# Kernel optimization log

Measured on AMD Instinct MI355X. Metric: run time of the kernel, lower is better.

Reference implementation:

```python
import jax, jax.numpy as jnp
import numpy as np
import math

B, S, E, HEAD = 4, 2048, 1024, 64  # num_heads=16 -> head_size = 1024//16


def setup_inputs() -> dict:
    key = jax.random.key(0)
    kx, kp, kq, kk, kv = jax.random.split(key, 5)
    std = math.sqrt(2.0 / (E + HEAD))
    return {
        "x": jax.random.normal(kx, (B, S, E), dtype=jnp.float32),
        "padding_mask": jax.random.randint(kp, (B, S), 0, 2, dtype=jnp.int32),
        "Wq": jax.random.normal(kq, (HEAD, E), dtype=jnp.float32) * std,
        "Wk": jax.random.normal(kk, (HEAD, E), dtype=jnp.float32) * std,
        "Wv": jax.random.normal(kv, (HEAD, E), dtype=jnp.float32) * std,
    }


def reference(x, padding_mask, Wq, Wk, Wv):
    # q,k,v: [B,S,head] via Linear (x @ W.T, no bias)
    q = jnp.einsum("bse,he->bsh", x, Wq)
    k = jnp.einsum("bse,he->bsh", x, Wk)
    v = jnp.einsum("bse,he->bsh", x, Wv)
    scores = jnp.einsum("bqh,bkh->bqk", q, k)  # [B,S,S]
    seq = x.shape[1]
    causal = jnp.tril(jnp.ones((seq, seq), dtype=jnp.float32))  # [S,S]
    mask = causal[None, :, :] * padding_mask.astype(jnp.float32)[:, None, :]  # [B,S,S]
    scores = jnp.where(mask == 0, jnp.float32(-1e9), scores)
    head_size = k.shape[-1]
    attn = jax.nn.softmax(scores / jnp.sqrt(jnp.float32(head_size)), axis=-1)
    return jnp.einsum("bqk,bkh->bqh", attn, v)
```

## Files before the change

### kernel.cpp

```cpp
#include <hip/hip_runtime.h>
#include <hip/hip_bf16.h>
#include <math.h>

#define B_ 4
#define S_ 2048
#define E_ 1024
#define H_ 64
#define NQT 32
#define SPLITS 8
#define TPS 4

typedef short bf16x8 __attribute__((ext_vector_type(8)));
typedef float f32x4 __attribute__((ext_vector_type(4)));
typedef unsigned short u16x8 __attribute__((ext_vector_type(8)));
typedef unsigned short u16x4 __attribute__((ext_vector_type(4)));

__device__ __forceinline__ unsigned short f2bf(float f){
    unsigned u = __builtin_bit_cast(unsigned, f);
    u += 0x7fffu + ((u >> 16) & 1u);
    return (unsigned short)(u >> 16);
}
__device__ __forceinline__ float bf2f(unsigned short h){
    return __builtin_bit_cast(float, ((unsigned)h) << 16);
}
#define MFMA16(a,b,c) __builtin_amdgcn_mfma_f32_16x16x32_bf16((a),(b),(c),0,0,0)

__global__ __launch_bounds__(256) void qkv_kernel(
    const float* __restrict__ x, const float* __restrict__ Wq,
    const float* __restrict__ Wk, const float* __restrict__ Wv,
    unsigned short* __restrict__ Qhi, unsigned short* __restrict__ Qlo,
    unsigned short* __restrict__ Khi, unsigned short* __restrict__ Klo,
    unsigned short* __restrict__ Vt)
{
    __shared__ unsigned short Ah[64*64], Al[64*64], Bh[64*64], Bl[64*64];
    const int m0 = blockIdx.x * 64;
    const int comp = blockIdx.y;
    const float* W = (comp==0) ? Wq : (comp==1) ? Wk : Wv;
    const int tid = threadIdx.x;
    const int lane = tid & 63, wv = tid >> 6, l15 = lane & 15, quad = lane >> 4;

    f32x4 acc[4];
    #pragma unroll
    for (int i=0;i<4;i++) acc[i] = f32x4{0.f,0.f,0.f,0.f};

    const int arow = tid >> 2;
    const int ag0  = (tid & 3) * 2;

    for (int k0 = 0; k0 < E_; k0 += 64) {
        const float* xs = x + (size_t)(m0 + arow)*E_ + k0 + ag0*8;
        float4 xa = ((const float4*)xs)[0];
        float4 xb = ((const float4*)xs)[1];
        float4 xc = ((const float4*)xs)[2];
        float4 xd = ((const float4*)xs)[3];
        const float* wsrc = W + (size_t)arow*E_ + k0 + ag0*8;
        float4 wa = ((const float4*)wsrc)[0];
        float4 wb = ((const float4*)wsrc)[1];
        float4 wc = ((const float4*)wsrc)[2];
        float4 wd = ((const float4*)wsrc)[3];
        __syncthreads();
        auto put = [&](unsigned short* hi_t, unsigned short* lo_t, int g, float4 p, float4 q2){
            u16x8 hv, lv;
            float vv[8] = {p.x,p.y,p.z,p.w,q2.x,q2.y,q2.z,q2.w};
            #pragma unroll
            for (int j=0;j<8;j++){ unsigned short h = f2bf(vv[j]); hv[j]=h; lv[j]=f2bf(vv[j]-bf2f(h)); }
            int idx = arow*8 + (g ^ (arow & 7));
            ((u16x8*)hi_t)[idx] = hv; ((u16x8*)lo_t)[idx] = lv;
        };
        put(Ah, Al, ag0,   xa, xb);
        put(Ah, Al, ag0+1, xc, xd);
        put(Bh, Bl, ag0,   wa, wb);
        put(Bh, Bl, ag0+1, wc, wd);
        __syncthreads();
        #pragma unroll
        for (int kk=0; kk<2; kk++){
            const int arw = wv*16 + l15;
            bf16x8 ah = ((const bf16x8*)Ah)[arw*8 + ((kk*4+quad) ^ (l15 & 7))];
            bf16x8 al = ((const bf16x8*)Al)[arw*8 + ((kk*4+quad) ^ (l15 & 7))];
            #pragma unroll
            for (int nt=0; nt<4; nt++){
                const int brw = nt*16 + l15;
                bf16x8 bh = ((const bf16x8*)Bh)[brw*8 + ((kk*4+quad) ^ (l15 & 7))];
                bf16x8 bl = ((const bf16x8*)Bl)[brw*8 + ((kk*4+quad) ^ (l15 & 7))];
                acc[nt] = MFMA16(ah, bh, acc[nt]);
                acc[nt] = MFMA16(ah, bl, acc[nt]);
                acc[nt] = MFMA16(al, bh, acc[nt]);
            }
        }
    }
    if (comp < 2) {
        unsigned short* dh = (comp==0) ? Qhi : Khi;
        unsigned short* dl = (comp==0) ? Qlo : Klo;
        #pragma unroll
        for (int nt=0; nt<4; nt++)
        #pragma unroll
        for (int r=0; r<4; r++){
            int row = m0 + wv*16 + quad*4 + r;
            float v = acc[nt][r];
            unsigned short h = f2bf(v);
            dh[(size_t)row*H_ + nt*16 + l15] = h;
            dl[(size_t)row*H_ + nt*16 + l15] = f2bf(v - bf2f(h));
        }
    } else {
        int b = m0 >> 11;
        int s0 = (m0 & (S_-1)) + wv*16 + quad*4;
        #pragma unroll
        for (int nt=0; nt<4; nt++){
            u16x4 pk;
            #pragma unroll
            for (int r=0;r<4;r++) pk[r] = f2bf(acc[nt][r]);
            *(u16x4*)(Vt + (size_t)b*H_*S_ + (size_t)(nt*16+l15)*S_ + s0) = pk;
        }
    }
}

__global__ __launch_bounds__(256) void meanv_kernel(const unsigned short* __restrict__ Vt,
                                                    float* __restrict__ meanV)
{
    int b = blockIdx.x >> 6, h = blockIdx.x & 63;
    const unsigned short* src = Vt + (size_t)b*H_*S_ + (size_t)h*S_;
    float sum = 0.f;
    for (int j = threadIdx.x; j < S_; j += 256) sum += bf2f(src[j]);
    #pragma unroll
    for (int m=32; m>=1; m>>=1) sum += __shfl_xor(sum, m);
    __shared__ float red[4];
    if ((threadIdx.x & 63) == 0) red[threadIdx.x >> 6] = sum;
    __syncthreads();
    if (threadIdx.x == 0) meanV[b*H_ + h] = (red[0]+red[1]+red[2]+red[3]) * (1.f/S_);
}

__global__ __launch_bounds__(256) void attn_kernel(
    const unsigned short* __restrict__ Qhi, const unsigned short* __restrict__ Qlo,
    const unsigned short* __restrict__ Khi, const unsigned short* __restrict__ Klo,
    const unsigned short* __restrict__ Vt, const int* __restrict__ pad,
    float* __restrict__ Opart, float* __restrict__ mpart, float* __restrict__ lpart)
{
    const int qt = blockIdx.x, b = blockIdx.y, sp = blockIdx.z;
    const int t0 = sp * TPS;
    if (t0 > qt) return;
    const int t1 = min(t0 + TPS, qt + 1);

    __shared__ unsigned short KtH[64*64], KtL[64*64], Vts[64*64];
    __shared__ unsigned short Ps[4][64*20];
    __shared__ int pad_s[64];

    const int tid = threadIdx.x, lane = tid & 63, wv = tid >> 6, l15 = lane & 15, quad = lane >> 4;
    const int role = tid >> 6, srow = tid & 63;

    const size_t qrow = (size_t)(b*S_ + qt*64 + wv*16 + l15);
    bf16x8 aqh0 = *(const bf16x8*)(Qhi + qrow*H_ + quad*8);
    bf16x8 aqh1 = *(const bf16x8*)(Qhi + qrow*H_ + 32 + quad*8);
    bf16x8 aql0 = *(const bf16x8*)(Qlo + qrow*H_ + quad*8);
    bf16x8 aql1 = *(const bf16x8*)(Qlo + qrow*H_ + 32 + quad*8);

    float m_i[4], l_i[4];
    f32x4 o[4];
    #pragma unroll
    for (int r=0;r<4;r++){ m_i[r] = -INFINITY; l_i[r] = 0.f; }
    #pragma unroll
    for (int i=0;i<4;i++) o[i] = f32x4{0.f,0.f,0.f,0.f};

    const int qg = qt*64 + wv*16 + quad*4;
    unsigned short* Pw = &Ps[wv][0];

    for (int t = t0; t < t1; ++t) {
        const int kb = t * 64;
        __syncthreads();
        if (role < 3) {
            const unsigned short* gs =
                (role==0) ? (Khi + ((size_t)(b*S_ + kb + srow))*H_) :
                (role==1) ? (Klo + ((size_t)(b*S_ + kb + srow))*H_) :
                            (Vt + (size_t)b*H_*S_ + (size_t)srow*S_ + kb);
            unsigned short* ld = (role==0) ? KtH : (role==1) ? KtL : Vts;
            #pragma unroll
            for (int i=0;i<8;i++){
                u16x8 d = ((const u16x8*)gs)[i];
                ((u16x8*)ld)[srow*8 + (i ^ (srow & 7))] = d;
            }
        } else {
            pad_s[srow] = pad[b*S_ + kb + srow];
        }
        __syncthreads();

        f32x4 s[4];
        #pragma unroll
        for (int nt=0; nt<4; nt++){
            const int krw = nt*16 + l15;
            bf16x8 bh0 = ((const bf16x8*)KtH)[krw*8 + ((quad)   ^ (l15 & 7))];
            bf16x8 bh1 = ((const bf16x8*)KtH)[krw*8 + ((4+quad) ^ (l15 & 7))];
            bf16x8 bl0 = ((const bf16x8*)KtL)[krw*8 + ((quad)   ^ (l15 & 7))];
            bf16x8 bl1 = ((const bf16x8*)KtL)[krw*8 + ((4+quad) ^ (l15 & 7))];
            f32x4 z = f32x4{0.f,0.f,0.f,0.f};
            z = MFMA16(aqh0, bh0, z);
            z = MFMA16(aqh1, bh1, z);
            z = MFMA16(aqh0, bl0, z);
            z = MFMA16(aqh1, bl1, z);
            z = MFMA16(aql0, bh0, z);
            z = MFMA16(aql1, bh1, z);
            s[nt] = z;
        }
        float rmax[4] = {-INFINITY,-INFINITY,-INFINITY,-INFINITY};
        #pragma unroll
        for (int nt=0; nt<4; nt++){
            const int kcol = nt*16 + l15;
            const int kg = kb + kcol;
            const int pv = pad_s[kcol];
            #pragma unroll
            for (int r=0;r<4;r++){
                bool ok = (kg <= qg + r) && (pv != 0);
                float v = ok ? s[nt][r]*0.125f : -1.25e8f;
                s[nt][r] = v;
                rmax[r] = fmaxf(rmax[r], v);
            }
        }
        #pragma unroll
        for (int msk=1; msk<=8; msk<<=1){
            #pragma unroll
            for (int r=0;r<4;r++) rmax[r] = fmaxf(rmax[r], __shfl_xor(rmax[r], msk));
        }
        float alpha[4];
        #pragma unroll
        for (int r=0;r<4;r++){
            float mn = fmaxf(m_i[r], rmax[r]);
            alpha[r] = __expf(m_i[r] - mn);
            m_i[r] = mn;
        }
        float rsum[4] = {0.f,0.f,0.f,0.f};
        #pragma unroll
        for (int nt=0; nt<4; nt++)
        #pragma unroll
        for (int r=0;r<4;r++){
            float p = __expf(s[nt][r] - m_i[r]);
            s[nt][r] = p;
            rsum[r] += p;
        }
        #pragma unroll
        for (int msk=1; msk<=8; msk<<=1){
            #pragma unroll
            for (int r=0;r<4;r++) rsum[r] += __shfl_xor(rsum[r], msk);
        }
        #pragma unroll
        for (int r=0;r<4;r++) l_i[r] = l_i[r]*alpha[r] + rsum[r];
        #pragma unroll
        for (int hnt=0; hnt<4; hnt++)
        #pragma unroll
        for (int r=0;r<4;r++) o[hnt][r] *= alpha[r];

        #pragma unroll
        for (int nt=0; nt<4; nt++){
            const int key = nt*16 + l15;
            u16x4 pk;
            #pragma unroll
            for (int r=0;r<4;r++) pk[r] = f2bf(s[nt][r]);
            *(u16x4*)(Pw + key*20 + quad*4) = pk;
        }
        #pragma unroll
        for (int ks=0; ks<2; ks++){
            bf16x8 ap;
            #pragma unroll
            for (int j=0;j<8;j++) ap[j] = (short)Pw[(ks*32 + quad*8 + j)*20 + l15];
            #pragma unroll
            for (int hnt=0; hnt<4; hnt++){
                bf16x8 bv = ((const bf16x8*)Vts)[(hnt*16+l15)*8 + ((ks*4+quad) ^ (l15 & 7))];
                o[hnt] = MFMA16(ap, bv, o[hnt]);
            }
        }
    }
    const size_t rbase = ((size_t)((b*NQT + qt)*SPLITS + sp))*64 + wv*16 + quad*4;
    if (l15 == 0) {
        #pragma unroll
        for (int r=0;r<4;r++){ mpart[rbase + r] = m_i[r]; lpart[rbase + r] = l_i[r]; }
    }
    #pragma unroll
    for (int hnt=0; hnt<4; hnt++)
    #pragma unroll
    for (int r=0;r<4;r++)
        Opart[(rbase + r)*H_ + hnt*16 + l15] = o[hnt][r];
}

__global__ __launch_bounds__(256) void combine_kernel(
    const float* __restrict__ Opart, const float* __restrict__ mpart,
    const float* __restrict__ lpart, const float* __restrict__ meanV,
    float* __restrict__ out)
{
    const int idx = blockIdx.x*256 + threadIdx.x;
    const int h = idx & 63;
    const int q = (idx >> 6) & (S_-1);
    const int b = idx >> 17;
    const int qt = q >> 6, r = q & 63;
    const int ns = (qt >> 2) + 1;
    const size_t rb = ((size_t)(b*NQT + qt)*SPLITS)*64 + r;
    float M = -INFINITY;
    for (int s2=0; s2<ns; s2++) M = fmaxf(M, mpart[rb + (size_t)s2*64]);
    float res;
    if (M == -1.25e8f) {
        res = meanV[b*H_ + h];
    } else {
        float L = 0.f, acc = 0.f;
        for (int s2=0; s2<ns; s2++){
            float mi = mpart[rb + (size_t)s2*64];
            float wgt = __expf(mi - M);
            L += wgt * lpart[rb + (size_t)s2*64];
            acc += wgt * Opart[(rb + (size_t)s2*64)*H_ + h];
        }
        res = acc / L;
    }
    out[idx] = res;
}

extern "C" void kernel_launch(void* const* d_in, const int* in_sizes, int n_in,
                              void* d_out, int out_size, void* d_ws, size_t ws_size,
                              hipStream_t stream)
{
    (void)in_sizes; (void)n_in; (void)out_size; (void)ws_size;
    const float* x  = (const float*)d_in[0];
    const int* pad  = (const int*)d_in[1];
    const float* Wq = (const float*)d_in[2];
    const float* Wk = (const float*)d_in[3];
    const float* Wv = (const float*)d_in[4];
    float* out = (float*)d_out;
    char* ws = (char*)d_ws;
    const size_t MB = 1u << 20;
    unsigned short* Qhi = (unsigned short*)(ws + 0*MB);
    unsigned short* Qlo = (unsigned short*)(ws + 1*MB);
    unsigned short* Khi = (unsigned short*)(ws + 2*MB);
    unsigned short* Klo = (unsigned short*)(ws + 3*MB);
    unsigned short* Vt  = (unsigned short*)(ws + 4*MB);
    float* Opart = (float*)(ws + 5*MB);
    float* mpart = (float*)(ws + 21*MB);
    float* lpart = (float*)(ws + 21*MB + (1u<<18));
    float* meanV = (float*)(ws + 21*MB + 2*(1u<<18));

    qkv_kernel<<<dim3(128,3), 256, 0, stream>>>(x, Wq, Wk, Wv, Qhi, Qlo, Khi, Klo, Vt);
    meanv_kernel<<<dim3(256), 256, 0, stream>>>(Vt, meanV);
    attn_kernel<<<dim3(NQT, B_, SPLITS), 256, 0, stream>>>(Qhi, Qlo, Khi, Klo, Vt, pad,
                                                           Opart, mpart, lpart);
    combine_kernel<<<dim3((B_*S_*H_)/256), 256, 0, stream>>>(Opart, mpart, lpart, meanV, out);
}
```

Before: 137.0 us.

## Fuse QKV projections per block, pre-split weights, use async LDS loads in attention

Adds a prep kernel that splits the weights into bf16 hi/lo once, and restructures the QKV kernel so each block computes Q, K and V for 32 rows, reading x only once and double-buffering its LDS tiles. The attention kernel now fills LDS with global_load_lds, replaces the shared padding array with a wave ballot mask, and transposes the MFMA operands so each lane owns one query row, which cuts the cross-lane reductions to two shuffles. The separate mean-V kernel is removed, and fully masked rows now compute the mean inline in the combine kernel. In exchange the combine kernel does a serial 2048-element loop on that rare path, and the LDS swizzles were dropped, which may add bank conflicts.

Result: slower. 164.4 us (+20.0%).

```diff
diff --git a/kernel.cpp b/kernel.cpp
--- a/kernel.cpp
+++ b/kernel.cpp
@@ -9,129 +9,145 @@
 #define NQT 32
 #define SPLITS 8
 #define TPS 4
+#define SENT (-1.25e8f)
 
 typedef short bf16x8 __attribute__((ext_vector_type(8)));
 typedef float f32x4 __attribute__((ext_vector_type(4)));
-typedef unsigned short u16x8 __attribute__((ext_vector_type(8)));
-typedef unsigned short u16x4 __attribute__((ext_vector_type(4)));
-
-__device__ __forceinline__ unsigned short f2bf(float f){
+typedef unsigned short U16;
+typedef U16 u16x8 __attribute__((ext_vector_type(8)));
+typedef U16 u16x4 __attribute__((ext_vector_type(4)));
+
+__device__ __forceinline__ U16 f2bf(float f){
     unsigned u = __builtin_bit_cast(unsigned, f);
     u += 0x7fffu + ((u >> 16) & 1u);
-    return (unsigned short)(u >> 16);
-}
-__device__ __forceinline__ float bf2f(unsigned short h){
+    return (U16)(u >> 16);
+}
+__device__ __forceinline__ float bf2f(U16 h){
     return __builtin_bit_cast(float, ((unsigned)h) << 16);
 }
 #define MFMA16(a,b,c) __builtin_amdgcn_mfma_f32_16x16x32_bf16((a),(b),(c),0,0,0)
 
+typedef const __attribute__((address_space(1))) void GvPtr;
+typedef __attribute__((address_space(3))) void LdsPtr;
+__device__ __forceinline__ void gload_lds16(const void* g, void* l){
+    __builtin_amdgcn_global_load_lds((GvPtr*)g, (LdsPtr*)l, 16, 0, 0);
+}
+
+__global__ __launch_bounds__(256) void prep_w(
+    const float* __restrict__ Wq, const float* __restrict__ Wk,
+    const float* __restrict__ Wv, U16* __restrict__ Whi, U16* __restrict__ Wlo)
+{
+    int i4 = (blockIdx.x*256 + threadIdx.x) * 4;
+    int c = i4 >> 16, rem = i4 & 65535;
+    const float* src = (c==0) ? Wq : (c==1) ? Wk : Wv;
+    float4 v = *(const float4*)(src + rem);
+    float a[4] = {v.x, v.y, v.z, v.w};
+    u16x4 hv, lv;
+    #pragma unroll
+    for (int j=0;j<4;j++){ U16 h = f2bf(a[j]); hv[j]=h; lv[j]=f2bf(a[j]-bf2f(h)); }
+    *(u16x4*)(Whi + i4) = hv;
+    *(u16x4*)(Wlo + i4) = lv;
+}
+
 __global__ __launch_bounds__(256) void qkv_kernel(
-    const float* __restrict__ x, const float* __restrict__ Wq,
-    const float* __restrict__ Wk, const float* __restrict__ Wv,
-    unsigned short* __restrict__ Qhi, unsigned short* __restrict__ Qlo,
-    unsigned short* __restrict__ Khi, unsigned short* __restrict__ Klo,
-    unsigned short* __restrict__ Vt)
-{
-    __shared__ unsigned short Ah[64*64], Al[64*64], Bh[64*64], Bl[64*64];
-    const int m0 = blockIdx.x * 64;
-    const int comp = blockIdx.y;
-    const float* W = (comp==0) ? Wq : (comp==1) ? Wk : Wv;
-    const int tid = threadIdx.x;
-    const int lane = tid & 63, wv = tid >> 6, l15 = lane & 15, quad = lane >> 4;
-
-    f32x4 acc[4];
-    #pragma unroll
-    for (int i=0;i<4;i++) acc[i] = f32x4{0.f,0.f,0.f,0.f};
-
-    const int arow = tid >> 2;
-    const int ag0  = (tid & 3) * 2;
-
+    const float* __restrict__ x, const U16* __restrict__ Whi_g,
+    const U16* __restrict__ Wlo_g,
+    U16* __restrict__ Qhi, U16* __restrict__ Qlo,
+    U16* __restrict__ Khi, U16* __restrict__ Klo, U16* __restrict__ Vt)
+{
+    __shared__ __align__(16) U16 Ah[2][32*64], Al[2][32*64];
+    const int m0 = blockIdx.x * 32;
+    const int tid = threadIdx.x, lane = tid & 63, wv = tid >> 6;
+    const int l15 = lane & 15, quad = lane >> 4;
+    const int arow = tid >> 3, ag = tid & 7;
+
+    f32x4 acc[3][2];
+    #pragma unroll
+    for (int c=0;c<3;c++)
+    #pragma unroll
+    for (int mt=0;mt<2;mt++) acc[c][mt] = f32x4{0.f,0.f,0.f,0.f};
+
+    {
+        const float* xs = x + (size_t)(m0 + arow)*E_ + ag*8;
+        float4 xa = ((const float4*)xs)[0], xb = ((const float4*)xs)[1];
+        float vv[8] = {xa.x,xa.y,xa.z,xa.w,xb.x,xb.y,xb.z,xb.w};
+        u16x8 hv, lv;
+        #pragma unroll
+        for (int j=0;j<8;j++){ U16 h = f2bf(vv[j]); hv[j]=h; lv[j]=f2bf(vv[j]-bf2f(h)); }
+        ((u16x8*)Ah[0])[arow*8 + ag] = hv;
+        ((u16x8*)Al[0])[arow*8 + ag] = lv;
+    }
+    __syncthreads();
+
+    int p = 0;
     for (int k0 = 0; k0 < E_; k0 += 64) {
-        const float* xs = x + (size_t)(m0 + arow)*E_ + k0 + ag0*8;
-        float4 xa = ((const float4*)xs)[0];
-        float4 xb = ((const float4*)xs)[1];
-        float4 xc = ((const float4*)xs)[2];
-        float4 xd = ((const float4*)xs)[3];
-        const float* wsrc = W + (size_t)arow*E_ + k0 + ag0*8;
-        float4 wa = ((const float4*)wsrc)[0];
-        float4 wb = ((const float4*)wsrc)[1];
-        float4 wc = ((const float4*)wsrc)[2];
-        float4 wd = ((const float4*)wsrc)[3];
+        float4 xa, xb;
+        const bool have = (k0 + 64 < E_);
+        if (have) {
+            const float* xs = x + (size_t)(m0 + arow)*E_ + k0 + 64 + ag*8;
+            xa = ((const float4*)xs)[0]; xb = ((const float4*)xs)[1];
+        }
+        bf16x8 bh[3][2], bl[3][2];
+        #pragma unroll
+        for (int c=0;c<3;c++)
+        #pragma unroll
+        for (int kk=0;kk<2;kk++){
+            const size_t wo = (size_t)c*65536 + (size_t)(wv*16 + l15)*E_ + k0 + kk*32 + quad*8;
+            bh[c][kk] = *(const bf16x8*)(Whi_g + wo);
+            bl[c][kk] = *(const bf16x8*)(Wlo_g + wo);
+        }
+        #pragma unroll
+        for (int kk=0;kk<2;kk++){
+            #pragma unroll
+            for (int mt=0;mt<2;mt++){
+                const int ai = (mt*16 + l15)*8 + kk*4 + quad;
+                bf16x8 ah = ((const bf16x8*)Ah[p])[ai];
+                bf16x8 al = ((const bf16x8*)Al[p])[ai];
+                #pragma unroll
+                for (int c=0;c<3;c++){
+                    acc[c][mt] = MFMA16(ah, bh[c][kk], acc[c][mt]);
+                    acc[c][mt] = MFMA16(ah, bl[c][kk], acc[c][mt]);
+                    acc[c][mt] = MFMA16(al, bh[c][kk], acc[c][mt]);
+                }
+            }
+        }
+        if (have) {
+            float vv[8] = {xa.x,xa.y,xa.z,xa.w,xb.x,xb.y,xb.z,xb.w};
+            u16x8 hv, lv;
+            #pragma unroll
+            for (int j=0;j<8;j++){ U16 h = f2bf(vv[j]); hv[j]=h; lv[j]=f2bf(vv[j]-bf2f(h)); }
+            ((u16x8*)Ah[p^1])[arow*8 + ag] = hv;
+            ((u16x8*)Al[p^1])[arow*8 + ag] = lv;
+        }
         __syncthreads();
-        auto put = [&](unsigned short* hi_t, unsigned short* lo_t, int g, float4 p, float4 q2){
-            u16x8 hv, lv;
-            float vv[8] = {p.x,p.y,p.z,p.w,q2.x,q2.y,q2.z,q2.w};
-            #pragma unroll
-            for (int j=0;j<8;j++){ unsigned short h = f2bf(vv[j]); hv[j]=h; lv[j]=f2bf(vv[j]-bf2f(h)); }
-            int idx = arow*8 + (g ^ (arow & 7));
-            ((u16x8*)hi_t)[idx] = hv; ((u16x8*)lo_t)[idx] = lv;
-        };
-        put(Ah, Al, ag0,   xa, xb);
-        put(Ah, Al, ag0+1, xc, xd);
-        put(Bh, Bl, ag0,   wa, wb);
-        put(Bh, Bl, ag0+1, wc, wd);
-        __syncthreads();
-        #pragma unroll
-        for (int kk=0; kk<2; kk++){
-            const int arw = wv*16 + l15;
-            bf16x8 ah = ((const bf16x8*)Ah)[arw*8 + ((kk*4+quad) ^ (l15 & 7))];
-            bf16x8 al = ((const bf16x8*)Al)[arw*8 + ((kk*4+quad) ^ (l15 & 7))];
-            #pragma unroll
-            for (int nt=0; nt<4; nt++){
-                const int brw = nt*16 + l15;
-                bf16x8 bh = ((const bf16x8*)Bh)[brw*8 + ((kk*4+quad) ^ (l15 & 7))];
-                bf16x8 bl = ((const bf16x8*)Bl)[brw*8 + ((kk*4+quad) ^ (l15 & 7))];
-                acc[nt] = MFMA16(ah, bh, acc[nt]);
-                acc[nt] = MFMA16(ah, bl, acc[nt]);
-                acc[nt] = MFMA16(al, bh, acc[nt]);
-            }
-        }
-    }
-    if (comp < 2) {
-        unsigned short* dh = (comp==0) ? Qhi : Khi;
-        unsigned short* dl = (comp==0) ? Qlo : Klo;
-        #pragma unroll
-        for (int nt=0; nt<4; nt++)
-        #pragma unroll
-        for (int r=0; r<4; r++){
-            int row = m0 + wv*16 + quad*4 + r;
-            float v = acc[nt][r];
-            unsigned short h = f2bf(v);
-            dh[(size_t)row*H_ + nt*16 + l15] = h;
-            dl[(size_t)row*H_ + nt*16 + l15] = f2bf(v - bf2f(h));
-        }
-    } else {
-        int b = m0 >> 11;
-        int s0 = (m0 & (S_-1)) + wv*16 + quad*4;
-        #pragma unroll
-        for (int nt=0; nt<4; nt++){
-            u16x4 pk;
-            #pragma unroll
-            for (int r=0;r<4;r++) pk[r] = f2bf(acc[nt][r]);
-            *(u16x4*)(Vt + (size_t)b*H_*S_ + (size_t)(nt*16+l15)*S_ + s0) = pk;
-        }
-    }
-}
-
-__global__ __launch_bounds__(256) void meanv_kernel(const unsigned short* __restrict__ Vt,
-                                                    float* __restrict__ meanV)
-{
-    int b = blockIdx.x >> 6, h = blockIdx.x & 63;
-    const unsigned short* src = Vt + (size_t)b*H_*S_ + (size_t)h*S_;
-    float sum = 0.f;
-    for (int j = threadIdx.x; j < S_; j += 256) sum += bf2f(src[j]);
-    #pragma unroll
-    for (int m=32; m>=1; m>>=1) sum += __shfl_xor(sum, m);
-    __shared__ float red[4];
-    if ((threadIdx.x & 63) == 0) red[threadIdx.x >> 6] = sum;
-    __syncthreads();
-    if (threadIdx.x == 0) meanV[b*H_ + h] = (red[0]+red[1]+red[2]+red[3]) * (1.f/S_);
+        p ^= 1;
+    }
+
+    const int h = wv*16 + l15;
+    #pragma unroll
+    for (int mt=0;mt<2;mt++){
+        const int row = m0 + mt*16 + quad*4;
+        #pragma unroll
+        for (int r=0;r<4;r++){
+            float vq = acc[0][mt][r]; U16 hq = f2bf(vq);
+            Qhi[(size_t)(row+r)*H_ + h] = hq;
+            Qlo[(size_t)(row+r)*H_ + h] = f2bf(vq - bf2f(hq));
+            float vk = acc[1][mt][r]; U16 hk = f2bf(vk);
+            Khi[(size_t)(row+r)*H_ + h] = hk;
+            Klo[(size_t)(row+r)*H_ + h] = f2bf(vk - bf2f(hk));
+        }
+        const int b = row >> 11, s0 = row & (S_-1);
+        u16x4 pk;
+        #pragma unroll
+        for (int r=0;r<4;r++) pk[r] = f2bf(acc[2][mt][r]);
+        *(u16x4*)(Vt + ((size_t)b*H_ + h)*S_ + s0) = pk;
+    }
 }
 
 __global__ __launch_bounds__(256) void attn_kernel(
-    const unsigned short* __restrict__ Qhi, const unsigned short* __restrict__ Qlo,
-    const unsigned short* __restrict__ Khi, const unsigned short* __restrict__ Klo,
-    const unsigned short* __restrict__ Vt, const int* __restrict__ pad,
+    const U16* __restrict__ Qhi, const U16* __restrict__ Qlo,
+    const U16* __restrict__ Khi, const U16* __restrict__ Klo,
+    const U16* __restrict__ Vt, const int* __restrict__ pad,
     float* __restrict__ Opart, float* __restrict__ mpart, float* __restrict__ lpart)
 {
     const int qt = blockIdx.x, b = blockIdx.y, sp = blockIdx.z;
@@ -139,147 +155,123 @@
     if (t0 > qt) return;
     const int t1 = min(t0 + TPS, qt + 1);
 
-    __shared__ unsigned short KtH[64*64], KtL[64*64], Vts[64*64];
-    __shared__ unsigned short Ps[4][64*20];
-    __shared__ int pad_s[64];
-
-    const int tid = threadIdx.x, lane = tid & 63, wv = tid >> 6, l15 = lane & 15, quad = lane >> 4;
-    const int role = tid >> 6, srow = tid & 63;
-
-    const size_t qrow = (size_t)(b*S_ + qt*64 + wv*16 + l15);
+    __shared__ __align__(16) U16 KtH[64*64], KtL[64*64], Vts[64*64];
+    __shared__ __align__(16) U16 Ps[4][16*80];
+
+    const int tid = threadIdx.x, lane = tid & 63, wv = tid >> 6;
+    const int l15 = lane & 15, quad = lane >> 4;
+
+    const size_t qrow = (size_t)b*S_ + qt*64 + wv*16 + l15;
     bf16x8 aqh0 = *(const bf16x8*)(Qhi + qrow*H_ + quad*8);
     bf16x8 aqh1 = *(const bf16x8*)(Qhi + qrow*H_ + 32 + quad*8);
     bf16x8 aql0 = *(const bf16x8*)(Qlo + qrow*H_ + quad*8);
     bf16x8 aql1 = *(const bf16x8*)(Qlo + qrow*H_ + 32 + quad*8);
 
-    float m_i[4], l_i[4];
+    float m_i = -INFINITY, l_i = 0.f;
     f32x4 o[4];
     #pragma unroll
-    for (int r=0;r<4;r++){ m_i[r] = -INFINITY; l_i[r] = 0.f; }
-    #pragma unroll
     for (int i=0;i<4;i++) o[i] = f32x4{0.f,0.f,0.f,0.f};
-
-    const int qg = qt*64 + wv*16 + quad*4;
-    unsigned short* Pw = &Ps[wv][0];
+    const int qg = qt*64 + wv*16 + l15;
+    U16* Pw = &Ps[wv][0];
 
     for (int t = t0; t < t1; ++t) {
         const int kb = t * 64;
         __syncthreads();
-        if (role < 3) {
-            const unsigned short* gs =
-                (role==0) ? (Khi + ((size_t)(b*S_ + kb + srow))*H_) :
-                (role==1) ? (Klo + ((size_t)(b*S_ + kb + srow))*H_) :
-                            (Vt + (size_t)b*H_*S_ + (size_t)srow*S_ + kb);
-            unsigned short* ld = (role==0) ? KtH : (role==1) ? KtL : Vts;
-            #pragma unroll
-            for (int i=0;i<8;i++){
-                u16x8 d = ((const u16x8*)gs)[i];
-                ((u16x8*)ld)[srow*8 + (i ^ (srow & 7))] = d;
+        {
+            const U16* kh = Khi + ((size_t)b*S_ + kb)*H_;
+            const U16* kl = Klo + ((size_t)b*S_ + kb)*H_;
+            #pragma unroll
+            for (int ch=0; ch<2; ++ch){
+                const int sb = wv*128 + ch*64;
+                const int slot = sb + lane;
+                gload_lds16(kh + (size_t)slot*8, (U16*)KtH + sb*8);
+                gload_lds16(kl + (size_t)slot*8, (U16*)KtL + sb*8);
+                const int vrow = slot >> 3, vg = slot & 7;
+                gload_lds16(Vt + ((size_t)b*H_ + vrow)*S_ + kb + vg*8, (U16*)Vts + sb*8);
             }
-        } else {
-            pad_s[srow] = pad[b*S_ + kb + srow];
-        }
+        }
+        const unsigned long long pm = __ballot(pad[(size_t)b*S_ + kb + lane] != 0);
         __syncthreads();
 
-        f32x4 s[4];
+        f32x4 z[4];
         #pragma unroll
         for (int nt=0; nt<4; nt++){
-            const int krw = nt*16 + l15;
-            bf16x8 bh0 = ((const bf16x8*)KtH)[krw*8 + ((quad)   ^ (l15 & 7))];
-            bf16x8 bh1 = ((const bf16x8*)KtH)[krw*8 + ((4+quad) ^ (l15 & 7))];
-            bf16x8 bl0 = ((const bf16x8*)KtL)[krw*8 + ((quad)   ^ (l15 & 7))];
-            bf16x8 bl1 = ((const bf16x8*)KtL)[krw*8 + ((4+quad) ^ (l15 & 7))];
-            f32x4 z = f32x4{0.f,0.f,0.f,0.f};
-            z = MFMA16(aqh0, bh0, z);
-            z = MFMA16(aqh1, bh1, z);
-            z = MFMA16(aqh0, bl0, z);
-            z = MFMA16(aqh1, bl1, z);
-            z = MFMA16(aql0, bh0, z);
-            z = MFMA16(aql1, bh1, z);
-            s[nt] = z;
-        }
-        float rmax[4] = {-INFINITY,-INFINITY,-INFINITY,-INFINITY};
+            const int kr = (nt*16 + l15)*8;
+            bf16x8 kh0 = ((const bf16x8*)KtH)[kr + quad];
+            bf16x8 kh1 = ((const bf16x8*)KtH)[kr + 4 + quad];
+            bf16x8 kl0 = ((const bf16x8*)KtL)[kr + quad];
+            bf16x8 kl1 = ((const bf16x8*)KtL)[kr + 4 + quad];
+            f32x4 zz = f32x4{0.f,0.f,0.f,0.f};
+            zz = MFMA16(kh0, aqh0, zz);
+            zz = MFMA16(kh1, aqh1, zz);
+            zz = MFMA16(kh0, aql0, zz);
+            zz = MFMA16(kh1, aql1, zz);
+            zz = MFMA16(kl0, aqh0, zz);
+            zz = MFMA16(kl1, aqh1, zz);
+            z[nt] = zz;
+        }
+        float rmax = -INFINITY;
         #pragma unroll
         for (int nt=0; nt<4; nt++){
-            const int kcol = nt*16 + l15;
-            const int kg = kb + kcol;
-            const int pv = pad_s[kcol];
+            const int rel = qg - kb - nt*16 - quad*4;
+            const unsigned mb = (unsigned)(pm >> (nt*16 + quad*4)) & 0xFu;
             #pragma unroll
             for (int r=0;r<4;r++){
-                bool ok = (kg <= qg + r) && (pv != 0);
-                float v = ok ? s[nt][r]*0.125f : -1.25e8f;
-                s[nt][r] = v;
-                rmax[r] = fmaxf(rmax[r], v);
+                const bool ok = (r <= rel) && ((mb >> r) & 1u);
+                const float v = ok ? z[nt][r]*0.125f : SENT;
+                z[nt][r] = v;
+                rmax = fmaxf(rmax, v);
             }
         }
-        #pragma unroll
-        for (int msk=1; msk<=8; msk<<=1){
-            #pragma unroll
-            for (int r=0;r<4;r++) rmax[r] = fmaxf(rmax[r], __shfl_xor(rmax[r], msk));
-        }
-        float alpha[4];
+        rmax = fmaxf(rmax, __shfl_xor(rmax, 16));
+        rmax = fmaxf(rmax, __shfl_xor(rmax, 32));
+        const float mn = fmaxf(m_i, rmax);
+        const float alpha = __expf(m_i - mn);
+        m_i = mn;
+        float rsum = 0.f;
+        #pragma unroll
+        for (int nt=0; nt<4; nt++)
         #pragma unroll
         for (int r=0;r<4;r++){
-            float mn = fmaxf(m_i[r], rmax[r]);
-            alpha[r] = __expf(m_i[r] - mn);
-            m_i[r] = mn;
-        }
-        float rsum[4] = {0.f,0.f,0.f,0.f};
+            const float pv = __expf(z[nt][r] - mn);
+            z[nt][r] = pv;
+            rsum += pv;
+        }
+        rsum += __shfl_xor(rsum, 16);
+        rsum += __shfl_xor(rsum, 32);
+        l_i = l_i*alpha + rsum;
         #pragma unroll
         for (int nt=0; nt<4; nt++)
         #pragma unroll
-        for (int r=0;r<4;r++){
-            float p = __expf(s[nt][r] - m_i[r]);
-            s[nt][r] = p;
-            rsum[r] += p;
-        }
-        #pragma unroll
-        for (int msk=1; msk<=8; msk<<=1){
-            #pragma unroll
-            for (int r=0;r<4;r++) rsum[r] += __shfl_xor(rsum[r], msk);
-        }
-        #pragma unroll
-        for (int r=0;r<4;r++) l_i[r] = l_i[r]*alpha[r] + rsum[r];
-        #pragma unroll
-        for (int hnt=0; hnt<4; hnt++)
-        #pragma unroll
-        for (int r=0;r<4;r++) o[hnt][r] *= alpha[r];
+        for (int r=0;r<4;r++) o[nt][r] *= alpha;
 
         #pragma unroll
         for (int nt=0; nt<4; nt++){
-            const int key = nt*16 + l15;
             u16x4 pk;
             #pragma unroll
-            for (int r=0;r<4;r++) pk[r] = f2bf(s[nt][r]);
-            *(u16x4*)(Pw + key*20 + quad*4) = pk;
+            for (int r=0;r<4;r++) pk[r] = f2bf(z[nt][r]);
+            *(u16x4*)(Pw + l15*80 + nt*16 + quad*4) = pk;
         }
         #pragma unroll
         for (int ks=0; ks<2; ks++){
-            bf16x8 ap;
-            #pragma unroll
-            for (int j=0;j<8;j++) ap[j] = (short)Pw[(ks*32 + quad*8 + j)*20 + l15];
-            #pragma unroll
-            for (int hnt=0; hnt<4; hnt++){
-                bf16x8 bv = ((const bf16x8*)Vts)[(hnt*16+l15)*8 + ((ks*4+quad) ^ (l15 & 7))];
-                o[hnt] = MFMA16(ap, bv, o[hnt]);
+            bf16x8 bp = *(const bf16x8*)(Pw + l15*80 + ks*32 + quad*8);
+            #pragma unroll
+            for (int nt=0; nt<4; nt++){
+                bf16x8 av = ((const bf16x8*)Vts)[(nt*16 + l15)*8 + ks*4 + quad];
+                o[nt] = MFMA16(av, bp, o[nt]);
             }
         }
     }
-    const size_t rbase = ((size_t)((b*NQT + qt)*SPLITS + sp))*64 + wv*16 + quad*4;
-    if (l15 == 0) {
-        #pragma unroll
-        for (int r=0;r<4;r++){ mpart[rbase + r] = m_i[r]; lpart[rbase + r] = l_i[r]; }
-    }
-    #pragma unroll
-    for (int hnt=0; hnt<4; hnt++)
-    #pragma unroll
-    for (int r=0;r<4;r++)
-        Opart[(rbase + r)*H_ + hnt*16 + l15] = o[hnt][r];
+    const size_t rbase = ((size_t)((b*NQT + qt)*SPLITS + sp))*64 + wv*16 + l15;
+    if (quad == 0) { mpart[rbase] = m_i; lpart[rbase] = l_i; }
+    #pragma unroll
+    for (int nt=0; nt<4; nt++)
+        *((f32x4*)(Opart + rbase*H_ + nt*16 + quad*4)) = o[nt];
 }
 
 __global__ __launch_bounds__(256) void combine_kernel(
     const float* __restrict__ Opart, const float* __restrict__ mpart,
-    const float* __restrict__ lpart, const float* __restrict__ meanV,
+    const float* __restrict__ lpart, const U16* __restrict__ Vt,
     float* __restrict__ out)
 {
     const int idx = blockIdx.x*256 + threadIdx.x;
@@ -292,17 +284,20 @@
     float M = -INFINITY;
     for (int s2=0; s2<ns; s2++) M = fmaxf(M, mpart[rb + (size_t)s2*64]);
     float res;
-    if (M == -1.25e8f) {
-        res = meanV[b*H_ + h];
+    if (M == SENT) {
+        const U16* vsrc = Vt + ((size_t)b*H_ + h)*S_;
+        float sm = 0.f;
+        for (int s=0; s<S_; ++s) sm += bf2f(vsrc[s]);
+        res = sm * (1.f/(float)S_);
     } else {
-        float L = 0.f, acc = 0.f;
+        float L = 0.f, accv = 0.f;
         for (int s2=0; s2<ns; s2++){
-            float mi = mpart[rb + (size_t)s2*64];
-            float wgt = __expf(mi - M);
-            L += wgt * lpart[rb + (size_t)s2*64];
-            acc += wgt * Opart[(rb + (size_t)s2*64)*H_ + h];
-        }
-        res = acc / L;
+            const float mi = mpart[rb + (size_t)s2*64];
+            const float w = __expf(mi - M);
+            L    += w * lpart[rb + (size_t)s2*64];
+            accv += w * Opart[(rb + (size_t)s2*64)*H_ + h];
+        }
+        res = accv / L;
     }
     out[idx] = res;
 }
@@ -320,19 +315,20 @@
     float* out = (float*)d_out;
     char* ws = (char*)d_ws;
     const size_t MB = 1u << 20;
-    unsigned short* Qhi = (unsigned short*)(ws + 0*MB);
-    unsigned short* Qlo = (unsigned short*)(ws + 1*MB);
-    unsigned short* Khi = (unsigned short*)(ws + 2*MB);
-    unsigned short* Klo = (unsigned short*)(ws + 3*MB);
-    unsigned short* Vt  = (unsigned short*)(ws + 4*MB);
-    float* Opart = (float*)(ws + 5*MB);
-    float* mpart = (float*)(ws + 21*MB);
-    float* lpart = (float*)(ws + 21*MB + (1u<<18));
-    float* meanV = (float*)(ws + 21*MB + 2*(1u<<18));
-
-    qkv_kernel<<<dim3(128,3), 256, 0, stream>>>(x, Wq, Wk, Wv, Qhi, Qlo, Khi, Klo, Vt);
-    meanv_kernel<<<dim3(256), 256, 0, stream>>>(Vt, meanV);
+    U16* Whi = (U16*)(ws);
+    U16* Wlo = (U16*)(ws + 393216);
+    U16* Qhi = (U16*)(ws + 1*MB);
+    U16* Qlo = (U16*)(ws + 2*MB);
+    U16* Khi = (U16*)(ws + 3*MB);
+    U16* Klo = (U16*)(ws + 4*MB);
+    U16* Vt  = (U16*)(ws + 5*MB);
+    float* Opart = (float*)(ws + 6*MB);
+    float* mpart = (float*)(ws + 22*MB);
+    float* lpart = (float*)(ws + 22*MB + (1u<<18));
+
+    prep_w<<<dim3(192), 256, 0, stream>>>(Wq, Wk, Wv, Whi, Wlo);
+    qkv_kernel<<<dim3(256), 256, 0, stream>>>(x, Whi, Wlo, Qhi, Qlo, Khi, Klo, Vt);
     attn_kernel<<<dim3(NQT, B_, SPLITS), 256, 0, stream>>>(Qhi, Qlo, Khi, Klo, Vt, pad,
                                                            Opart, mpart, lpart);
-    combine_kernel<<<dim3((B_*S_*H_)/256), 256, 0, stream>>>(Opart, mpart, lpart, meanV, out);
-}
+    combine_kernel<<<dim3((B_*S_*H_)/256), 256, 0, stream>>>(Opart, mpart, lpart, Vt, out);
+}
```
